# Optimization experiments

Hardware: AMD Instinct MI355X
Metric: run time of the kernel (lower is better)

Reference implementation:

```python
import jax, jax.numpy as jnp
import numpy as np

N = 50000      # nodes
E = 800000     # edges (avg degree 16)
G = 256        # graphs in batch
IN = 128       # in_channels
H = 256        # hidden_channels
L = 4          # num_layers


def setup_inputs() -> dict:
    key = jax.random.key(0)
    ks = jax.random.split(key, 16)
    x = jax.random.normal(ks[0], (N, IN), dtype=jnp.float32)
    edge_index = jax.random.randint(ks[1], (2, E), 0, N, dtype=jnp.int64)
    batch = jnp.sort(jax.random.randint(ks[2], (N,), 0, G, dtype=jnp.int64))
    s_in = 1.0 / np.sqrt(IN)
    s_h = 1.0 / np.sqrt(H)
    return {
        "x": x,
        "edge_index": edge_index,
        "batch": batch,
        "w1_0": jax.random.normal(ks[3], (IN, H), jnp.float32) * s_in,
        "b1_0": jnp.zeros((H,), jnp.float32),
        "w2_0": jax.random.normal(ks[4], (H, H), jnp.float32) * s_h,
        "b2_0": jnp.zeros((H,), jnp.float32),
        "w1s": jax.random.normal(ks[5], (L - 1, H, H), jnp.float32) * s_h,
        "b1s": jnp.zeros((L - 1, H), jnp.float32),
        "w2s": jax.random.normal(ks[6], (L - 1, H, H), jnp.float32) * s_h,
        "b2s": jnp.zeros((L - 1, H), jnp.float32),
    }


def reference(x, edge_index, batch, w1_0, b1_0, w2_0, b2_0, w1s, b1s, w2s, b2s):
    n_nodes = x.shape[0]
    src, dst = edge_index[0], edge_index[1]

    def gin_layer(h, w1, b1, w2, b2):
        # scatter-add neighbor aggregation: out[i] = sum_{(j->i)} h[j]
        agg = jax.ops.segment_sum(h[src], dst, num_segments=n_nodes)
        z = h + agg  # GIN with eps = 0: (1+eps)*x + aggr
        z = jax.nn.relu(z @ w1 + b1) @ w2 + b2  # MLP: Linear-ReLU-Linear
        return jax.nn.relu(z)  # outer F.relu in forward

    h = gin_layer(x, w1_0, b1_0, w2_0, b2_0)
    for i in range(L - 1):  # small fixed layer loop
        h = gin_layer(h, w1s[i], b1s[i], w2s[i], b2s[i])

    # global_add_pool: per-graph segment sum -> [G, H]
    return jax.ops.segment_sum(h, batch, num_segments=G)
```

## Files before the change

### kernel.cpp

```cpp
#include <hip/hip_runtime.h>
#include <hip/hip_bf16.h>

#define NN 50000
#define NE 800000
#define NG 256
#define CIN 128
#define CH 256
#define CAP 64

typedef unsigned short u16;
typedef unsigned int u32;
typedef __attribute__((ext_vector_type(8))) short short8;
typedef __attribute__((ext_vector_type(8))) unsigned short ushort8;
typedef __attribute__((ext_vector_type(4))) float f32x4;

__device__ __forceinline__ float bf2f(u16 u) { return __uint_as_float(((u32)u) << 16); }
__device__ __forceinline__ u16 f2bf(float f) {
    u32 u = __float_as_uint(f);
    return (u16)((u + 0x7fffu + ((u >> 16) & 1u)) >> 16);
}

__global__ void k_prep(const float* __restrict__ x, u16* __restrict__ xb,
                       const float* __restrict__ w1_0, const float* __restrict__ w2_0,
                       const float* __restrict__ w1s, const float* __restrict__ w2s,
                       u16* __restrict__ Wp, int* __restrict__ deg,
                       float* __restrict__ outf,
                       u16* __restrict__ Hb, u16* __restrict__ Tb) {
    int t = blockIdx.x * 256 + threadIdx.x;
    if (t < NN) deg[t] = 0;
    if (t < NG * CH) outf[t] = 0.f;
    if (t < CH) {
        Hb[(size_t)NN * CH + t] = 0;
        Tb[(size_t)NN * CH + t] = 0;
        if (t < CIN) xb[(size_t)NN * CIN + t] = 0;
    }
    if (t < NN * CIN / 4) {
        float4 v = ((const float4*)x)[t];
        ushort4 o; o.x = f2bf(v.x); o.y = f2bf(v.y); o.z = f2bf(v.z); o.w = f2bf(v.w);
        ((ushort4*)xb)[t] = o;
    }
    if (t < CIN * CH + 7 * CH * CH) {
        const float* Wsrc; int rem;
        if (t < CIN * CH) { Wsrc = w1_0; rem = t; }
        else {
            int o = t - CIN * CH;
            int m = o >> 16; rem = o & 65535;
            Wsrc = (m == 0) ? w2_0
                 : (m <= 3) ? w1s + (size_t)(m - 1) * 65536
                            : w2s + (size_t)(m - 4) * 65536;
        }
        int j = rem & 7, lane = (rem >> 3) & 63, nt = (rem >> 9) & 15, kb = rem >> 13;
        int k = kb * 32 + ((lane >> 4) << 3) + j;
        int nc = nt * 16 + (lane & 15);
        Wp[t] = f2bf(Wsrc[k * CH + nc]);
    }
}

__global__ void k_build(const int* __restrict__ dst, const int* __restrict__ src,
                        int* __restrict__ deg, int* __restrict__ col) {
    int e = blockIdx.x * 256 + threadIdx.x;
    if (e < NE) {
        int d = dst[e];
        int pos = atomicAdd(&deg[d], 1);
        col[d * CAP + pos] = src[e];
    }
}

#define ZS 264
template <int K1, bool POOL>
__global__ __launch_bounds__(256, 7) void k_layer(const u16* __restrict__ G,
                                                  const int* __restrict__ deg,
                                                  const int* __restrict__ col,
                                                  const u16* __restrict__ Wp1,
                                                  const float* __restrict__ b1,
                                                  const u16* __restrict__ Wp2,
                                                  const float* __restrict__ b2,
                                                  u16* __restrict__ out,
                                                  const int* __restrict__ batchp,
                                                  float* __restrict__ outf) {
    __shared__ __align__(16) u16 zs[32 * ZS];
    const int tid = threadIdx.x;
    const int wave = tid >> 6, lane = tid & 63;
    const int quad = lane >> 4, l16 = lane & 15;
    const int m0 = blockIdx.x * 32;

    constexpr int LPR = K1 / 8;
    constexpr int RPG = 64 / LPR;
    const int sub = lane / LPR;
    const int c0 = (lane % LPR) * 8;
    for (int g = 0; g < 8; g += RPG) {
        int lr = wave * 8 + g + sub;
        int r = m0 + lr; if (r >= NN) r = NN - 1;
        const u16* base = G + c0;
        float a[8];
        ushort8 sv = *(const ushort8*)(base + (size_t)r * K1);
#pragma unroll
        for (int i = 0; i < 8; i++) a[i] = bf2f(sv[i]);
        int beg = r * CAP, end = beg + deg[r];
        for (int e = beg; e < end; e += 8) {
            int4 ca = *(const int4*)(col + e);
            int4 cb = *(const int4*)(col + e + 4);
            int idx[8] = {ca.x, ca.y, ca.z, ca.w, cb.x, cb.y, cb.z, cb.w};
#pragma unroll
            for (int u = 0; u < 8; u++)
                if (e + u >= end) idx[u] = NN;
            ushort8 v[8];
#pragma unroll
            for (int u = 0; u < 8; u++)
                v[u] = *(const ushort8*)(base + (size_t)idx[u] * K1);
#pragma unroll
            for (int u = 0; u < 8; u++)
#pragma unroll
                for (int i = 0; i < 8; i++) a[i] += bf2f(v[u][i]);
        }
        ushort8 o;
#pragma unroll
        for (int i = 0; i < 8; i++) o[i] = f2bf(a[i]);
        *(ushort8*)(zs + lr * ZS + c0) = o;
    }
    __syncthreads();

    f32x4 acc[2][4];
#pragma unroll
    for (int ri = 0; ri < 2; ri++)
#pragma unroll
        for (int nj = 0; nj < 4; nj++) acc[ri][nj] = (f32x4){0.f, 0.f, 0.f, 0.f};

    const u16* w1b = Wp1 + (wave * 4) * 512 + lane * 8;
    const u16* w2b = Wp2 + (wave * 4) * 512 + lane * 8;
    constexpr int KB1 = K1 / 32;
    short8 b_cur[4], b_nxt[4];
#pragma unroll
    for (int nj = 0; nj < 4; nj++) b_cur[nj] = *(const short8*)(w1b + nj * 512);

#pragma unroll
    for (int kb = 0; kb < KB1; kb++) {
        int kn = (kb + 1 < KB1) ? (kb + 1) : kb;
#pragma unroll
        for (int nj = 0; nj < 4; nj++)
            b_nxt[nj] = *(const short8*)(w1b + kn * 8192 + nj * 512);
        short8 a[2];
#pragma unroll
        for (int ri = 0; ri < 2; ri++)
            a[ri] = *(const short8*)(zs + (ri * 16 + l16) * ZS + kb * 32 + quad * 8);
#pragma unroll
        for (int nj = 0; nj < 4; nj++)
#pragma unroll
            for (int ri = 0; ri < 2; ri++)
                acc[ri][nj] = __builtin_amdgcn_mfma_f32_16x16x32_bf16(a[ri], b_cur[nj], acc[ri][nj], 0, 0, 0);
#pragma unroll
        for (int nj = 0; nj < 4; nj++) b_cur[nj] = b_nxt[nj];
    }

    short8 b2_cur[4];
#pragma unroll
    for (int nj = 0; nj < 4; nj++) b2_cur[nj] = *(const short8*)(w2b + nj * 512);

    __syncthreads();

#pragma unroll
    for (int nj = 0; nj < 4; nj++) {
        int cc = wave * 64 + nj * 16 + l16;
        float bv = b1[cc];
#pragma unroll
        for (int ri = 0; ri < 2; ri++) {
            f32x4 v = acc[ri][nj];
#pragma unroll
            for (int j = 0; j < 4; j++)
                zs[(ri * 16 + quad * 4 + j) * ZS + cc] = f2bf(fmaxf(v[j] + bv, 0.f));
        }
    }
    __syncthreads();

#pragma unroll
    for (int ri = 0; ri < 2; ri++)
#pragma unroll
        for (int nj = 0; nj < 4; nj++) acc[ri][nj] = (f32x4){0.f, 0.f, 0.f, 0.f};

#pragma unroll
    for (int kb = 0; kb < 8; kb++) {
        int kn = (kb + 1 < 8) ? (kb + 1) : kb;
#pragma unroll
        for (int nj = 0; nj < 4; nj++)
            b_nxt[nj] = *(const short8*)(w2b + kn * 8192 + nj * 512);
        short8 a[2];
#pragma unroll
        for (int ri = 0; ri < 2; ri++)
            a[ri] = *(const short8*)(zs + (ri * 16 + l16) * ZS + kb * 32 + quad * 8);
#pragma unroll
        for (int nj = 0; nj < 4; nj++)
#pragma unroll
            for (int ri = 0; ri < 2; ri++)
                acc[ri][nj] = __builtin_amdgcn_mfma_f32_16x16x32_bf16(a[ri], b2_cur[nj], acc[ri][nj], 0, 0, 0);
#pragma unroll
        for (int nj = 0; nj < 4; nj++) b2_cur[nj] = b_nxt[nj];
    }
    __syncthreads();

#pragma unroll
    for (int nj = 0; nj < 4; nj++) {
        int cc = wave * 64 + nj * 16 + l16;
        float bv = b2[cc];
#pragma unroll
        for (int ri = 0; ri < 2; ri++) {
            f32x4 v = acc[ri][nj];
#pragma unroll
            for (int j = 0; j < 4; j++)
                zs[(ri * 16 + quad * 4 + j) * ZS + cc] = f2bf(fmaxf(v[j] + bv, 0.f));
        }
    }
    __syncthreads();

    if (!POOL) {
        int row = tid >> 3, cb = (tid & 7) * 32;
        if (m0 + row < NN) {
            uint4* dst = (uint4*)(out + (size_t)(m0 + row) * CH + cb);
            const u16* srcp = zs + row * ZS + cb;
#pragma unroll
            for (int c = 0; c < 4; c++) dst[c] = *(const uint4*)(srcp + c * 8);
        }
    } else {
        int c = tid;
        float acc2 = 0.f;
        int cur_g = batchp[m0];
        for (int row = 0; row < 32; row++) {
            int r = m0 + row;
            if (r >= NN) break;
            int g = batchp[r];
            if (g != cur_g) {
                atomicAdd(&outf[cur_g * CH + c], acc2);
                acc2 = 0.f; cur_g = g;
            }
            acc2 += bf2f(zs[row * ZS + c]);
        }
        atomicAdd(&outf[cur_g * CH + c], acc2);
    }
}

extern "C" void kernel_launch(void* const* d_in, const int* in_sizes, int n_in,
                              void* d_out, int out_size, void* d_ws, size_t ws_size,
                              hipStream_t stream) {
    const float* x     = (const float*)d_in[0];
    const int*   ei    = (const int*)d_in[1];
    const int*   batch = (const int*)d_in[2];
    const float* w1_0  = (const float*)d_in[3];
    const float* b1_0  = (const float*)d_in[4];
    const float* w2_0  = (const float*)d_in[5];
    const float* b2_0  = (const float*)d_in[6];
    const float* w1s   = (const float*)d_in[7];
    const float* b1s   = (const float*)d_in[8];
    const float* w2s   = (const float*)d_in[9];
    const float* b2s   = (const float*)d_in[10];
    float* out = (float*)d_out;

    char* p = (char*)d_ws;
    u16* Hb  = (u16*)p; p += (size_t)(NN + 1) * CH * 2;
    u16* Tb  = (u16*)p; p += (size_t)(NN + 1) * CH * 2;
    u16* xb  = (u16*)p; p += (size_t)(NN + 1) * CIN * 2;
    u16* WpA = (u16*)p; p += (size_t)(CIN * CH + 7 * CH * CH) * 2;
    int* deg = (int*)p; p += (size_t)NN * 4;
    int* col = (int*)p; p += (size_t)NN * CAP * 4;

    u16* Wp1_0 = WpA;
    u16* Wp2_0 = Wp1_0 + CIN * CH;
    u16* Wp1sA = Wp2_0 + CH * CH;
    u16* Wp2sA = Wp1sA + 3 * CH * CH;

    const int* srcv = ei;
    const int* dstv = ei + NE;

    hipLaunchKernelGGL(k_prep, dim3((NN * CIN / 4 + 255) / 256), dim3(256), 0, stream,
                       x, xb, w1_0, w2_0, w1s, w2s, WpA, deg, out, Hb, Tb);

    hipLaunchKernelGGL(k_build, dim3((NE + 255) / 256), dim3(256), 0, stream,
                       dstv, srcv, deg, col);

    int layerBlocks = (NN + 31) / 32;

    hipLaunchKernelGGL((k_layer<128, false>), dim3(layerBlocks), dim3(256), 0, stream,
                       xb, deg, col, Wp1_0, b1_0, Wp2_0, b2_0, Hb, batch, out);
    hipLaunchKernelGGL((k_layer<256, false>), dim3(layerBlocks), dim3(256), 0, stream,
                       Hb, deg, col, Wp1sA, b1s, Wp2sA, b2s, Tb, batch, out);
    hipLaunchKernelGGL((k_layer<256, false>), dim3(layerBlocks), dim3(256), 0, stream,
                       Tb, deg, col, Wp1sA + (size_t)CH * CH, b1s + CH,
                       Wp2sA + (size_t)CH * CH, b2s + CH, Hb, batch, out);
    hipLaunchKernelGGL((k_layer<256, true>), dim3(layerBlocks), dim3(256), 0, stream,
                       Hb, deg, col, Wp1sA + (size_t)2 * CH * CH, b1s + 2 * CH,
                       Wp2sA + (size_t)2 * CH * CH, b2s + 2 * CH, (u16*)nullptr, batch, out);
}
```

Baseline: 423.6 us.

## Quantize hidden activations to uint8 with per-row scale for neighbor gathers

Each layer now also writes a uint8 copy of its post-ReLU output, scaled per row by the row max, plus a float scale per row. The next layer's neighbor aggregation reads these 8-bit rows and scales instead of bf16 rows, which halves the bytes moved by the random gather. The self term still comes from the bf16 copy. The cost is extra quantization work and writes in the epilogue, a slightly lower occupancy bound, and reduced precision in the aggregated sums.

Measured after the change: 400.9 us. 5.4% less time.

```diff
diff --git a/kernel.cpp b/kernel.cpp
--- a/kernel.cpp
+++ b/kernel.cpp
@@ -10,6 +10,7 @@
 
 typedef unsigned short u16;
 typedef unsigned int u32;
+typedef unsigned char u8;
 typedef __attribute__((ext_vector_type(8))) short short8;
 typedef __attribute__((ext_vector_type(8))) unsigned short ushort8;
 typedef __attribute__((ext_vector_type(4))) float f32x4;
@@ -25,15 +26,12 @@
                        const float* __restrict__ w1s, const float* __restrict__ w2s,
                        u16* __restrict__ Wp, int* __restrict__ deg,
                        float* __restrict__ outf,
-                       u16* __restrict__ Hb, u16* __restrict__ Tb) {
+                       float* __restrict__ S0, float* __restrict__ S1) {
     int t = blockIdx.x * 256 + threadIdx.x;
     if (t < NN) deg[t] = 0;
     if (t < NG * CH) outf[t] = 0.f;
-    if (t < CH) {
-        Hb[(size_t)NN * CH + t] = 0;
-        Tb[(size_t)NN * CH + t] = 0;
-        if (t < CIN) xb[(size_t)NN * CIN + t] = 0;
-    }
+    if (t < CIN) xb[(size_t)NN * CIN + t] = 0;
+    if (t == 0) { S0[NN] = 0.f; S1[NN] = 0.f; }
     if (t < NN * CIN / 4) {
         float4 v = ((const float4*)x)[t];
         ushort4 o; o.x = f2bf(v.x); o.y = f2bf(v.y); o.z = f2bf(v.z); o.w = f2bf(v.w);
@@ -67,15 +65,19 @@
 }
 
 #define ZS 264
-template <int K1, bool POOL>
-__global__ __launch_bounds__(256, 7) void k_layer(const u16* __restrict__ G,
+template <int K1, bool QIN, bool QOUT, bool POOL>
+__global__ __launch_bounds__(256, 6) void k_layer(const u16* __restrict__ G,
                                                   const int* __restrict__ deg,
                                                   const int* __restrict__ col,
+                                                  const u8* __restrict__ Qin,
+                                                  const float* __restrict__ Sin,
                                                   const u16* __restrict__ Wp1,
                                                   const float* __restrict__ b1,
                                                   const u16* __restrict__ Wp2,
                                                   const float* __restrict__ b2,
                                                   u16* __restrict__ out,
+                                                  u8* __restrict__ Qout,
+                                                  float* __restrict__ Sout,
                                                   const int* __restrict__ batchp,
                                                   float* __restrict__ outf) {
     __shared__ __align__(16) u16 zs[32 * ZS];
@@ -84,39 +86,84 @@
     const int quad = lane >> 4, l16 = lane & 15;
     const int m0 = blockIdx.x * 32;
 
-    constexpr int LPR = K1 / 8;
-    constexpr int RPG = 64 / LPR;
-    const int sub = lane / LPR;
-    const int c0 = (lane % LPR) * 8;
-    for (int g = 0; g < 8; g += RPG) {
-        int lr = wave * 8 + g + sub;
-        int r = m0 + lr; if (r >= NN) r = NN - 1;
-        const u16* base = G + c0;
-        float a[8];
-        ushort8 sv = *(const ushort8*)(base + (size_t)r * K1);
-#pragma unroll
-        for (int i = 0; i < 8; i++) a[i] = bf2f(sv[i]);
-        int beg = r * CAP, end = beg + deg[r];
-        for (int e = beg; e < end; e += 8) {
-            int4 ca = *(const int4*)(col + e);
-            int4 cb = *(const int4*)(col + e + 4);
-            int idx[8] = {ca.x, ca.y, ca.z, ca.w, cb.x, cb.y, cb.z, cb.w};
-#pragma unroll
-            for (int u = 0; u < 8; u++)
-                if (e + u >= end) idx[u] = NN;
-            ushort8 v[8];
-#pragma unroll
-            for (int u = 0; u < 8; u++)
-                v[u] = *(const ushort8*)(base + (size_t)idx[u] * K1);
-#pragma unroll
-            for (int u = 0; u < 8; u++)
-#pragma unroll
-                for (int i = 0; i < 8; i++) a[i] += bf2f(v[u][i]);
-        }
-        ushort8 o;
-#pragma unroll
-        for (int i = 0; i < 8; i++) o[i] = f2bf(a[i]);
-        *(ushort8*)(zs + lr * ZS + c0) = o;
+    if (!QIN) {
+        constexpr int LPR = K1 / 8;
+        constexpr int RPG = 64 / LPR;
+        const int sub = lane / LPR;
+        const int c0 = (lane % LPR) * 8;
+        for (int g = 0; g < 8; g += RPG) {
+            int lr = wave * 8 + g + sub;
+            int r = m0 + lr; if (r >= NN) r = NN - 1;
+            const u16* base = G + c0;
+            float a[8];
+            ushort8 sv = *(const ushort8*)(base + (size_t)r * K1);
+#pragma unroll
+            for (int i = 0; i < 8; i++) a[i] = bf2f(sv[i]);
+            int beg = r * CAP, end = beg + deg[r];
+            for (int e = beg; e < end; e += 8) {
+                int4 ca = *(const int4*)(col + e);
+                int4 cb = *(const int4*)(col + e + 4);
+                int idx[8] = {ca.x, ca.y, ca.z, ca.w, cb.x, cb.y, cb.z, cb.w};
+#pragma unroll
+                for (int u = 0; u < 8; u++)
+                    if (e + u >= end) idx[u] = NN;
+                ushort8 v[8];
+#pragma unroll
+                for (int u = 0; u < 8; u++)
+                    v[u] = *(const ushort8*)(base + (size_t)idx[u] * K1);
+#pragma unroll
+                for (int u = 0; u < 8; u++)
+#pragma unroll
+                    for (int i = 0; i < 8; i++) a[i] += bf2f(v[u][i]);
+            }
+            ushort8 o;
+#pragma unroll
+            for (int i = 0; i < 8; i++) o[i] = f2bf(a[i]);
+            *(ushort8*)(zs + lr * ZS + c0) = o;
+        }
+    } else {
+        const int sub = lane >> 4;
+        const int c0 = (lane & 15) * 16;
+        for (int g = 0; g < 8; g += 4) {
+            int lr = wave * 8 + g + sub;
+            int r = m0 + lr; if (r >= NN) r = NN - 1;
+            float a[16];
+            const u16* sp = G + (size_t)r * CH + c0;
+            ushort8 s0v = *(const ushort8*)sp;
+            ushort8 s1v = *(const ushort8*)(sp + 8);
+#pragma unroll
+            for (int i = 0; i < 8; i++) { a[i] = bf2f(s0v[i]); a[8 + i] = bf2f(s1v[i]); }
+            int beg = r * CAP, end = beg + deg[r];
+            for (int e = beg; e < end; e += 4) {
+                int4 ca = *(const int4*)(col + e);
+                int idx[4] = {ca.x, ca.y, ca.z, ca.w};
+#pragma unroll
+                for (int u = 0; u < 4; u++)
+                    if (e + u >= end) idx[u] = NN;
+                uint4 qv[4]; float sc[4];
+#pragma unroll
+                for (int u = 0; u < 4; u++) {
+                    qv[u] = *(const uint4*)(Qin + (size_t)idx[u] * CH + c0);
+                    sc[u] = Sin[idx[u]];
+                }
+#pragma unroll
+                for (int u = 0; u < 4; u++) {
+#pragma unroll
+                    for (int d = 0; d < 4; d++) {
+                        u32 w = ((const u32*)&qv[u])[d];
+                        a[d * 4 + 0] += sc[u] * (float)(w & 0xffu);
+                        a[d * 4 + 1] += sc[u] * (float)((w >> 8) & 0xffu);
+                        a[d * 4 + 2] += sc[u] * (float)((w >> 16) & 0xffu);
+                        a[d * 4 + 3] += sc[u] * (float)(w >> 24);
+                    }
+                }
+            }
+            ushort8 o0, o1;
+#pragma unroll
+            for (int i = 0; i < 8; i++) { o0[i] = f2bf(a[i]); o1[i] = f2bf(a[8 + i]); }
+            *(ushort8*)(zs + lr * ZS + c0) = o0;
+            *(ushort8*)(zs + lr * ZS + c0 + 8) = o1;
+        }
     }
     __syncthreads();
 
@@ -213,11 +260,34 @@
 
     if (!POOL) {
         int row = tid >> 3, cb = (tid & 7) * 32;
-        if (m0 + row < NN) {
-            uint4* dst = (uint4*)(out + (size_t)(m0 + row) * CH + cb);
+        int r = m0 + row;
+        if (r < NN) {
+            uint4* dst = (uint4*)(out + (size_t)r * CH + cb);
             const u16* srcp = zs + row * ZS + cb;
 #pragma unroll
             for (int c = 0; c < 4; c++) dst[c] = *(const uint4*)(srcp + c * 8);
+            if (QOUT) {
+                float vloc[32]; float mx = 0.f;
+#pragma unroll
+                for (int c = 0; c < 32; c++) { vloc[c] = bf2f(srcp[c]); mx = fmaxf(mx, vloc[c]); }
+                mx = fmaxf(mx, __shfl_xor(mx, 1));
+                mx = fmaxf(mx, __shfl_xor(mx, 2));
+                mx = fmaxf(mx, __shfl_xor(mx, 4));
+                float inv = mx > 0.f ? 255.f / mx : 0.f;
+                u32 qw[8];
+#pragma unroll
+                for (int d = 0; d < 8; d++) {
+                    u32 q0 = (u32)(vloc[d * 4 + 0] * inv + 0.5f);
+                    u32 q1 = (u32)(vloc[d * 4 + 1] * inv + 0.5f);
+                    u32 q2 = (u32)(vloc[d * 4 + 2] * inv + 0.5f);
+                    u32 q3 = (u32)(vloc[d * 4 + 3] * inv + 0.5f);
+                    qw[d] = q0 | (q1 << 8) | (q2 << 16) | (q3 << 24);
+                }
+                uint4* qdst = (uint4*)(Qout + (size_t)r * CH + cb);
+                qdst[0] = *(const uint4*)&qw[0];
+                qdst[1] = *(const uint4*)&qw[4];
+                if ((tid & 7) == 0) Sout[r] = mx * (1.f / 255.f);
+            }
         }
     } else {
         int c = tid;
@@ -260,6 +330,10 @@
     u16* WpA = (u16*)p; p += (size_t)(CIN * CH + 7 * CH * CH) * 2;
     int* deg = (int*)p; p += (size_t)NN * 4;
     int* col = (int*)p; p += (size_t)NN * CAP * 4;
+    u8*  Q0  = (u8*)p;  p += (size_t)(NN + 1) * CH;
+    u8*  Q1  = (u8*)p;  p += (size_t)(NN + 1) * CH;
+    float* S0 = (float*)p; p += (size_t)(NN + 1) * 4;
+    float* S1 = (float*)p; p += (size_t)(NN + 1) * 4;
 
     u16* Wp1_0 = WpA;
     u16* Wp2_0 = Wp1_0 + CIN * CH;
@@ -270,21 +344,26 @@
     const int* dstv = ei + NE;
 
     hipLaunchKernelGGL(k_prep, dim3((NN * CIN / 4 + 255) / 256), dim3(256), 0, stream,
-                       x, xb, w1_0, w2_0, w1s, w2s, WpA, deg, out, Hb, Tb);
+                       x, xb, w1_0, w2_0, w1s, w2s, WpA, deg, out, S0, S1);
 
     hipLaunchKernelGGL(k_build, dim3((NE + 255) / 256), dim3(256), 0, stream,
                        dstv, srcv, deg, col);
 
     int layerBlocks = (NN + 31) / 32;
 
-    hipLaunchKernelGGL((k_layer<128, false>), dim3(layerBlocks), dim3(256), 0, stream,
-                       xb, deg, col, Wp1_0, b1_0, Wp2_0, b2_0, Hb, batch, out);
-    hipLaunchKernelGGL((k_layer<256, false>), dim3(layerBlocks), dim3(256), 0, stream,
-                       Hb, deg, col, Wp1sA, b1s, Wp2sA, b2s, Tb, batch, out);
-    hipLaunchKernelGGL((k_layer<256, false>), dim3(layerBlocks), dim3(256), 0, stream,
-                       Tb, deg, col, Wp1sA + (size_t)CH * CH, b1s + CH,
-                       Wp2sA + (size_t)CH * CH, b2s + CH, Hb, batch, out);
-    hipLaunchKernelGGL((k_layer<256, true>), dim3(layerBlocks), dim3(256), 0, stream,
-                       Hb, deg, col, Wp1sA + (size_t)2 * CH * CH, b1s + 2 * CH,
-                       Wp2sA + (size_t)2 * CH * CH, b2s + 2 * CH, (u16*)nullptr, batch, out);
-}
+    hipLaunchKernelGGL((k_layer<128, false, true, false>), dim3(layerBlocks), dim3(256), 0, stream,
+                       xb, deg, col, (const u8*)nullptr, (const float*)nullptr,
+                       Wp1_0, b1_0, Wp2_0, b2_0, Hb, Q0, S0, batch, out);
+    hipLaunchKernelGGL((k_layer<256, true, true, false>), dim3(layerBlocks), dim3(256), 0, stream,
+                       Hb, deg, col, Q0, S0,
+                       Wp1sA, b1s, Wp2sA, b2s, Tb, Q1, S1, batch, out);
+    hipLaunchKernelGGL((k_layer<256, true, true, false>), dim3(layerBlocks), dim3(256), 0, stream,
+                       Tb, deg, col, Q1, S1,
+                       Wp1sA + (size_t)CH * CH, b1s + CH,
+                       Wp2sA + (size_t)CH * CH, b2s + CH, Hb, Q0, S0, batch, out);
+    hipLaunchKernelGGL((k_layer<256, true, false, true>), dim3(layerBlocks), dim3(256), 0, stream,
+                       Hb, deg, col, Q0, S0,
+                       Wp1sA + (size_t)2 * CH * CH, b1s + 2 * CH,
+                       Wp2sA + (size_t)2 * CH * CH, b2s + 2 * CH,
+                       (u16*)nullptr, (u8*)nullptr, (float*)nullptr, batch, out);
+}
```
